# Kernel tuning notes

Hardware: AMD Instinct MI355X
Metric: run time of the kernel (lower is better)

Reference implementation:

```python
import jax, jax.numpy as jnp
import numpy as np
from jax import lax

NQ = 5  # qubits
NL = 3  # circuit layers


def conv2d(x, w, b):
    y = lax.conv_general_dilated(x, w, (1, 1), 'SAME',
                                 dimension_numbers=('NCHW', 'OIHW', 'NCHW'))
    return y + b[None, :, None, None]


def batchnorm(x, g, b, eps=1e-5):
    # training-mode batch statistics over (N,H,W), matching nn.BatchNorm2d in train()
    mu = x.mean((0, 2, 3), keepdims=True)
    var = x.var((0, 2, 3), keepdims=True)
    return g[None, :, None, None] * (x - mu) * lax.rsqrt(var + eps) + b[None, :, None, None]


def maxpool2(x):
    return lax.reduce_window(x, -jnp.inf, lax.max, (1, 1, 2, 2), (1, 1, 2, 2), 'VALID')


def _apply_1q(state, U, w):
    # state: (2,)*NQ, wire w is axis w (PennyLane default.qubit ordering)
    s = jnp.tensordot(U, state, axes=([1], [w]))
    return jnp.moveaxis(s, 0, w)


def _cnot(state, c, t):
    s0 = jnp.take(state, 0, axis=c)
    s1 = jnp.take(state, 1, axis=c)
    ta = t if t < c else t - 1
    s1 = jnp.flip(s1, axis=ta)  # X on target when control=1
    return jnp.stack([s0, s1], axis=c)


def _rx(t):
    c, s = jnp.cos(t / 2), jnp.sin(t / 2)
    return jnp.array([[c, -1j * s], [-1j * s, c]], dtype=jnp.complex64)


def _ry(t):
    c, s = jnp.cos(t / 2), jnp.sin(t / 2)
    return jnp.array([[c, -s], [s, c]], dtype=jnp.complex64)


def _rz(t):
    e = jnp.exp(-1j * t / 2)
    z = jnp.zeros((), jnp.complex64)
    return jnp.array([[e, z], [z, jnp.conj(e)]], dtype=jnp.complex64)


def quantum_circuit(inputs, weights):
    # inputs: (5,), weights: (30,)  -> scalar <Z0 Z1 Z2>
    state = jnp.zeros((2,) * NQ, jnp.complex64).at[(0,) * NQ].set(1.0)
    npl = NQ * 2  # weights per layer = 10
    nw = weights.shape[0]
    for l in range(NL):
        for i in range(NQ):
            state = _apply_1q(state, _rx(inputs[i]), i)
        for i in range(NQ):
            state = _apply_1q(state, _ry(weights[(l * npl + i) % nw]), i)
            state = _apply_1q(state, _rz(weights[(l * npl + i + NQ) % nw]), i)
        for i in range(NQ - 1):
            state = _cnot(state, i, i + 1)
        state = _cnot(state, NQ - 1, 0)
    probs = jnp.abs(state) ** 2
    z = jnp.array([1.0, -1.0], jnp.float32)
    sign = z[:, None, None] * z[None, :, None] * z[None, None, :]  # Z on wires 0,1,2
    return jnp.sum(probs * sign[:, :, :, None, None])


def setup_inputs() -> dict:
    key = jax.random.key(0)
    ks = jax.random.split(key, 12)
    d = {}
    d['x'] = jax.random.normal(ks[0], (256, 1, 224, 224), jnp.float32)
    d['conv1_w'] = jax.random.normal(ks[1], (16, 1, 3, 3), jnp.float32) * 0.1
    d['conv1_b'] = jnp.zeros((16,), jnp.float32)
    d['bn1_g'] = jnp.ones((16,), jnp.float32)
    d['bn1_b'] = jnp.zeros((16,), jnp.float32)
    d['conv2_w'] = jax.random.normal(ks[2], (32, 16, 3, 3), jnp.float32) * 0.05
    d['conv2_b'] = jnp.zeros((32,), jnp.float32)
    d['bn2_g'] = jnp.ones((32,), jnp.float32)
    d['bn2_b'] = jnp.zeros((32,), jnp.float32)
    d['conv3_w'] = jax.random.normal(ks[3], (64, 32, 3, 3), jnp.float32) * 0.05
    d['conv3_b'] = jnp.zeros((64,), jnp.float32)
    d['bn3_g'] = jnp.ones((64,), jnp.float32)
    d['bn3_b'] = jnp.zeros((64,), jnp.float32)
    d['fc1_w'] = jax.random.normal(ks[4], (64, 5), jnp.float32) * 0.1   # (in,out)
    d['fc1_b'] = jnp.zeros((5,), jnp.float32)
    d['ln_g'] = jnp.ones((5,), jnp.float32)
    d['ln_b'] = jnp.zeros((5,), jnp.float32)
    d['q_params'] = jax.random.uniform(ks[5], (30,), jnp.float32)
    d['fc2_w'] = jax.random.normal(ks[6], (1, 32), jnp.float32) * 0.5
    d['fc2_b'] = jnp.zeros((32,), jnp.float32)
    d['fc3_w'] = jax.random.normal(ks[7], (32, 2), jnp.float32) * 0.2
    d['fc3_b'] = jnp.zeros((2,), jnp.float32)
    return d


def reference(x, conv1_w, conv1_b, bn1_g, bn1_b, conv2_w, conv2_b, bn2_g, bn2_b,
              conv3_w, conv3_b, bn3_g, bn3_b, fc1_w, fc1_b, ln_g, ln_b,
              q_params, fc2_w, fc2_b, fc3_w, fc3_b):
    h = maxpool2(jax.nn.relu(batchnorm(conv2d(x, conv1_w, conv1_b), bn1_g, bn1_b)))
    h = maxpool2(jax.nn.relu(batchnorm(conv2d(h, conv2_w, conv2_b), bn2_g, bn2_b)))
    h = maxpool2(jax.nn.relu(batchnorm(conv2d(h, conv3_w, conv3_b), bn3_g, bn3_b)))
    # dropout is identity in eval; adaptive avg pool (1,1) + flatten
    h = h.mean((2, 3))                    # (B, 64)
    h = h @ fc1_w + fc1_b                 # (B, 5)
    mu = h.mean(-1, keepdims=True)
    var = h.var(-1, keepdims=True)
    h = ln_g * (h - mu) * lax.rsqrt(var + 1e-5) + ln_b
    q = jax.vmap(lambda inp: quantum_circuit(inp, q_params))(h)  # (B,)
    q = q[:, None].astype(jnp.float32)    # (B, 1)
    h2 = jax.nn.relu(q @ fc2_w + fc2_b)   # (B, 32)
    logits = h2 @ fc3_w + fc3_b           # (B, 2)
    return jax.nn.log_softmax(logits, axis=1)
```

## Files before the change

kernel.cpp:

```cpp
#include <hip/hip_runtime.h>
#include <hip/hip_bf16.h>


typedef _Float16 f16;
typedef _Float16 f16x2 __attribute__((ext_vector_type(2)));
typedef _Float16 f16x4 __attribute__((ext_vector_type(4)));
typedef _Float16 f16x8 __attribute__((ext_vector_type(8)));
typedef float f32x4 __attribute__((ext_vector_type(4)));
typedef float f32x16 __attribute__((ext_vector_type(16)));

#define DEV static __device__ __forceinline__

DEV float wave_sum(float v) {
#pragma unroll
  for (int off = 32; off > 0; off >>= 1) v += __shfl_xor(v, off, 64);
  return v;
}

__global__ __launch_bounds__(256) void repack(const float* __restrict__ w2,
                                              const float* __restrict__ w3,
                                              f16* __restrict__ Bt2,
                                              f16* __restrict__ Bt3) {
  int t = blockIdx.x * 256 + threadIdx.x;
  int T = gridDim.x * 256;
  for (int i = t; i < 32 * 168; i += T) {
    int oc = i / 168, kk = i - oc * 168;
    float v = 0.f;
    if (kk < 144) {
      int tap = kk >> 4, ic = kk & 15;
      v = w2[(oc * 16 + ic) * 9 + tap];
    }
    Bt2[i] = (f16)v;
  }
  for (int i = t; i < 64 * 296; i += T) {
    int oc = i / 296, kk = i - oc * 296;
    float v = 0.f;
    if (kk < 288) {
      int tap = kk / 32, ic = kk & 31;
      v = w3[(oc * 32 + ic) * 9 + tap];
    }
    Bt3[i] = (f16)v;
  }
}

__global__ __launch_bounds__(64) void finalize(const float* __restrict__ banks,
                                               const float* __restrict__ g,
                                               const float* __restrict__ b,
                                               float* __restrict__ scsh, int C,
                                               float inv_n) {
  int c = blockIdx.x, bk = threadIdx.x;
  float s = banks[bk * 2 * C + c];
  float qq = banks[bk * 2 * C + C + c];
  s = wave_sum(s);
  qq = wave_sum(qq);
  if (bk == 0) {
    float mean = s * inv_n;
    float var = qq * inv_n - mean * mean;
    float sc = g[c] * rsqrtf(var + 1e-5f);
    scsh[c] = sc;
    scsh[C + c] = b[c] - mean * sc;
  }
}

__global__ __launch_bounds__(256) void l1_mfma32(const float* __restrict__ x,
                                                 const float* __restrict__ w1,
                                                 float* __restrict__ banks,
                                                 f16* __restrict__ h1raw) {
  __shared__ f16 xA[18 * 240];
  __shared__ f16 xB[18 * 240];
  __shared__ f16 lrow[4 * 3616];
  __shared__ float lstat[32];
  int bid = blockIdx.x;
  int n = bid / 14, band = bid - n * 14;
  int y0 = band * 16;
  int t = threadIdx.x;
  if (t < 32) lstat[t] = 0.f;
  for (int i = t; i < 1008; i += 256) {
    int r = i / 56, k = i - r * 56;
    int y = y0 - 1 + r;
    float4 v = make_float4(0.f, 0.f, 0.f, 0.f);
    if ((unsigned)y < 224u)
      v = *(const float4*)(x + ((size_t)(n * 224 + y)) * 224 + k * 4);
    f16 h0 = (f16)v.x, h1 = (f16)v.y, h2 = (f16)v.z, h3 = (f16)v.w;
    f16* pa = xA + r * 240 + 4 * k + 1;
    pa[0] = h0; pa[1] = h1; pa[2] = h2; pa[3] = h3;
    f16x4 pk = {h0, h1, h2, h3};
    *(f16x4*)(xB + r * 240 + 4 * k) = pk;
  }
  if (t < 18) {
    xA[t * 240 + 0] = (f16)0.f;
    xA[t * 240 + 225] = (f16)0.f;
    xA[t * 240 + 226] = (f16)0.f;
    xB[t * 240 + 224] = (f16)0.f;
    xB[t * 240 + 225] = (f16)0.f;
  }
  __syncthreads();

  int wave = t >> 6, lane = t & 63;
  int g = lane >> 5, m32 = lane & 31;
  int oc = m32 & 15, s = m32 >> 4;

  f16x8 b;
#pragma unroll
  for (int j = 0; j < 8; j++) {
    int ky = 2 * g + (j >> 2), kx = j & 3;
    int kys = ky - s;
    float wv = 0.f;
    if (kx < 3 && kys >= 0 && kys < 3) wv = w1[oc * 9 + kys * 3 + kx];
    b[j] = (f16)wv;
  }

  const f16* abase = (m32 & 1) ? (xB + (m32 - 1)) : (xA + m32);
  f16* myrow = lrow + wave * 3616;
  f16* mrow = myrow + s * 1808;
  f32x16 zero16;
#pragma unroll
  for (int r = 0; r < 16; r++) zero16[r] = 0.f;
  const int bp[8] = {0, 1, 4, 5, 8, 9, 12, 13};
  float ssum = 0.f, ssq = 0.f;

  for (int rp = wave; rp < 8; rp += 4) {
    int r0 = 2 * rp + 2 * g;
    const f16* rbase = abase + r0 * 240;
#pragma unroll
    for (int xt = 0; xt < 7; xt++) {
      const f16* p0 = rbase + xt * 32;
      f16x2 v0 = *(const f16x2*)(p0);
      f16x2 v1 = *(const f16x2*)(p0 + 2);
      f16x2 v2 = *(const f16x2*)(p0 + 240);
      f16x2 v3 = *(const f16x2*)(p0 + 242);
      f16x8 a = {v0[0], v0[1], v1[0], v1[1], v2[0], v2[1], v3[0], v3[1]};
      f32x16 acc = __builtin_amdgcn_mfma_f32_32x32x16_f16(a, b, zero16, 0, 0, 0);
#pragma unroll
      for (int r = 0; r < 16; r++) {
        float v = acc[r];
        ssum += v;
        ssq += v * v;
      }
#pragma unroll
      for (int i = 0; i < 8; i++) {
        float pm = fmaxf(acc[2 * i], acc[2 * i + 1]);
        int pxp = xt * 16 + bp[i] + 2 * g;
        mrow[pxp * 16 + oc] = (f16)pm;
      }
    }
    int ph = band * 8 + rp;
    f16* gdst = h1raw + ((size_t)(n * 112) + ph) * 112 * 16;
    for (int i = lane; i < 224; i += 64) {
      f16x8 va = *(const f16x8*)(myrow + i * 8);
      f16x8 vb = *(const f16x8*)(myrow + 1808 + i * 8);
#pragma unroll
      for (int k = 0; k < 8; k++) va[k] = (va[k] > vb[k]) ? va[k] : vb[k];
      *(f16x8*)(gdst + i * 8) = va;
    }
  }
  ssum += __shfl_xor(ssum, 16, 64);
  ssum += __shfl_xor(ssum, 32, 64);
  ssq += __shfl_xor(ssq, 16, 64);
  ssq += __shfl_xor(ssq, 32, 64);
  if (lane < 16) {
    atomicAdd(&lstat[oc], ssum);
    atomicAdd(&lstat[16 + oc], ssq);
  }
  __syncthreads();
  if (t < 32) atomicAdd(&banks[(bid & 63) * 32 + t], lstat[t]);
}

__global__ __launch_bounds__(256, 2) void l2_gemm(
    const f16* __restrict__ h1, const f16* __restrict__ Btg,
    const float* __restrict__ scsh1, f16* __restrict__ p2,
    float* __restrict__ banks) {
  extern __shared__ char smem[];
  f16* lin0 = (f16*)smem;
  f16* lin1 = (f16*)(smem + 32832);
  f16* lpool = (f16*)(smem + 65664);
  float* lstat = (float*)(smem + 72832);
  int bid = blockIdx.x;
  int n = bid / 7, sb = bid - n * 7;
  int t = threadIdx.x;
  int wave = t >> 6, lane = t & 63, q = lane >> 4, wi = lane & 15;
  const int icq = (q & 1) * 8;

  f16x8 breg0[5], breg1[5];
#pragma unroll
  for (int j = 0; j < 5; j++) {
    breg0[j] = *(const f16x8*)(Btg + wi * 168 + j * 32 + q * 8);
    breg1[j] = *(const f16x8*)(Btg + (16 + wi) * 168 + j * 32 + q * 8);
  }

  f16x8 L[6];
  {
    int gb4 = sb * 16;
#pragma unroll
    for (int k = 0; k < 6; k++) {
      int i = t + k * 256;
      f16x8 v = {0, 0, 0, 0, 0, 0, 0, 0};
      if (i < 1344) {
        int r = i / 224, c = i - r * 224;
        int y = gb4 + r - 1;
        if ((unsigned)y < 112u)
          v = *(const f16x8*)(h1 + ((size_t)(n * 112 + y)) * 112 * 16 + c * 8);
      }
      L[k] = v;
    }
  }
  __builtin_amdgcn_sched_barrier(0);
  if (t < 64) lstat[t] = 0.f;
  if (t < 48) {
    f16* dst = (t < 24) ? lin0 : lin1;
    int tt = (t < 24) ? t : t - 24;
    int r = tt >> 2, k2 = tt & 3;
    f16x8 z = {0, 0, 0, 0, 0, 0, 0, 0};
    int pos = (k2 < 2) ? 0 : 113;
    *(f16x8*)(dst + (r * 114 + pos) * 24 + (k2 & 1) * 8) = z;
  }
  {
    int gb4 = sb * 16;
#pragma unroll
    for (int k = 0; k < 6; k++) {
      int i = t + k * 256;
      if (i < 1344) {
        int r = i / 224, c = i - r * 224;
        int y = gb4 + r - 1;
        f16x8 o = {0, 0, 0, 0, 0, 0, 0, 0};
        if ((unsigned)y < 112u) {
          f16x8 xv = L[k];
          int ch0 = (c & 1) * 8;
#pragma unroll
          for (int e = 0; e < 8; e++) {
            float f = (float)xv[e] * scsh1[ch0 + e] + scsh1[16 + ch0 + e];
            o[e] = (f16)fmaxf(f, 0.f);
          }
        }
        *(f16x8*)(lin0 + (r * 114 + 1 + (c >> 1)) * 24 + (c & 1) * 8) = o;
      }
    }
  }
  __syncthreads();

  float tS0 = 0.f, tQ0 = 0.f, tS1 = 0.f, tQ1 = 0.f;
  f16* cur = lin0;
  f16* nxt = lin1;

  for (int b = 0; b < 4; b++) {
    int gb = sb * 4 + b;
    if (b < 3) {
      int gb4 = (gb + 1) * 4;
#pragma unroll
      for (int k = 0; k < 6; k++) {
        int i = t + k * 256;
        f16x8 v = {0, 0, 0, 0, 0, 0, 0, 0};
        if (i < 1344) {
          int r = i / 224, c = i - r * 224;
          int y = gb4 + r - 1;
          if ((unsigned)y < 112u)
            v = *(const f16x8*)(h1 +
                                ((size_t)(n * 112 + y)) * 112 * 16 + c * 8);
        }
        L[k] = v;
      }
      __builtin_amdgcn_sched_barrier(0);
    }

    f32x4 acc[7][2];
#pragma unroll
    for (int f = 0; f < 7; f++)
#pragma unroll
      for (int nf = 0; nf < 2; nf++)
#pragma unroll
        for (int r = 0; r < 4; r++) acc[f][nf][r] = 0.f;

#pragma unroll
    for (int j = 0; j < 5; j++) {
      const int tA = 2 * j, tB = 2 * j + 1;
      const int kyA = tA / 3, kxA = tA % 3;
      const int kyB = (tB < 9) ? tB / 3 : 0, kxB = (tB < 9) ? tB % 3 : 0;
      bool hiq = (q >= 2);
      int ky = hiq ? kyB : kyA;
      int kx = hiq ? kxB : kxA;
      const f16* aptr0 = cur + ((wave + ky) * 114 + wi + kx) * 24 + icq;
      f16x8 b0 = breg0[j];
      f16x8 b1 = breg1[j];
#pragma unroll
      for (int f = 0; f < 7; f++) {
        f16x8 a = *(const f16x8*)(aptr0 + f * 384);
        acc[f][0] =
            __builtin_amdgcn_mfma_f32_16x16x32_f16(a, b0, acc[f][0], 0, 0, 0);
        acc[f][1] =
            __builtin_amdgcn_mfma_f32_16x16x32_f16(a, b1, acc[f][1], 0, 0, 0);
      }
    }

#pragma unroll
    for (int f = 0; f < 7; f++)
#pragma unroll
      for (int r = 0; r < 4; r++) {
        float v0 = acc[f][0][r], v1 = acc[f][1][r];
        tS0 += v0; tQ0 += v0 * v0;
        tS1 += v1; tQ1 += v1 * v1;
      }

    if (wave & 1) {
#pragma unroll
      for (int f = 0; f < 7; f++)
#pragma unroll
        for (int nf = 0; nf < 2; nf++) {
          int ch = nf * 16 + wi;
          int pc0 = f * 8 + q * 2;
          float m0 = fmaxf(acc[f][nf][0], acc[f][nf][1]);
          float m1 = fmaxf(acc[f][nf][2], acc[f][nf][3]);
          lpool[((wave >> 1) * 56 + pc0) * 32 + ch] = (f16)m0;
          lpool[((wave >> 1) * 56 + pc0 + 1) * 32 + ch] = (f16)m1;
        }
    }

    if (b < 3) {
      int gb4 = (gb + 1) * 4;
#pragma unroll
      for (int k = 0; k < 6; k++) {
        int i = t + k * 256;
        if (i < 1344) {
          int r = i / 224, c = i - r * 224;
          int y = gb4 + r - 1;
          f16x8 o = {0, 0, 0, 0, 0, 0, 0, 0};
          if ((unsigned)y < 112u) {
            f16x8 xv = L[k];
            int ch0 = (c & 1) * 8;
#pragma unroll
            for (int e = 0; e < 8; e++) {
              float f = (float)xv[e] * scsh1[ch0 + e] + scsh1[16 + ch0 + e];
              o[e] = (f16)fmaxf(f, 0.f);
            }
          }
          *(f16x8*)(nxt + (r * 114 + 1 + (c >> 1)) * 24 + (c & 1) * 8) = o;
        }
      }
    }
    __syncthreads();

    if (!(wave & 1)) {
      int ph = gb * 2 + (wave >> 1);
#pragma unroll
      for (int f = 0; f < 7; f++)
#pragma unroll
        for (int nf = 0; nf < 2; nf++) {
          int ch = nf * 16 + wi;
          int pc0 = f * 8 + q * 2;
          float m0 = fmaxf(acc[f][nf][0], acc[f][nf][1]);
          float m1 = fmaxf(acc[f][nf][2], acc[f][nf][3]);
          m0 = fmaxf(m0, (float)lpool[((wave >> 1) * 56 + pc0) * 32 + ch]);
          m1 = fmaxf(m1, (float)lpool[((wave >> 1) * 56 + pc0 + 1) * 32 + ch]);
          size_t ob = (((size_t)n * 56 + ph) * 56) * 32;
          p2[ob + (size_t)pc0 * 32 + ch] = (f16)m0;
          p2[ob + (size_t)(pc0 + 1) * 32 + ch] = (f16)m1;
        }
    }
    __syncthreads();

    f16* tmpp = cur; cur = nxt; nxt = tmpp;
  }

  tS0 += __shfl_xor(tS0, 16, 64); tS0 += __shfl_xor(tS0, 32, 64);
  tQ0 += __shfl_xor(tQ0, 16, 64); tQ0 += __shfl_xor(tQ0, 32, 64);
  tS1 += __shfl_xor(tS1, 16, 64); tS1 += __shfl_xor(tS1, 32, 64);
  tQ1 += __shfl_xor(tQ1, 16, 64); tQ1 += __shfl_xor(tQ1, 32, 64);
  if (q == 0) {
    atomicAdd(&lstat[wi], tS0);
    atomicAdd(&lstat[16 + wi], tS1);
    atomicAdd(&lstat[32 + wi], tQ0);
    atomicAdd(&lstat[48 + wi], tQ1);
  }
  __syncthreads();
  if (t < 64) {
    int i = t >> 5, c = t & 31;
    atomicAdd(&banks[(bid & 63) * 64 + i * 32 + c], lstat[i * 32 + c]);
  }
}

__global__ __launch_bounds__(256) void l3_gemm(const f16* __restrict__ p2,
                                               const f16* __restrict__ Btg,
                                               const float* __restrict__ scsh2,
                                               f16* __restrict__ p3,
                                               float* __restrict__ banks) {
  extern __shared__ char smem[];
  f16* lin = (f16*)smem;
  float* lstat = (float*)(smem + 27840);
  f16* lpool = (f16*)smem;
  int bx = blockIdx.x;
  int n = bx / 14, band = bx - n * 14, h0 = band * 4;
  int t = threadIdx.x;
  int wave = t >> 6, lane = t & 63, q = lane >> 4, wi = lane & 15;
  int mhalf = wave & 1, nfpair = wave >> 1;
  f16x8 breg0[9], breg1[9];
#pragma unroll
  for (int j = 0; j < 9; j++) {
    breg0[j] = *(const f16x8*)(Btg + (nfpair * 32 + wi) * 296 + j * 32 + q * 8);
    breg1[j] =
        *(const f16x8*)(Btg + (nfpair * 32 + 16 + wi) * 296 + j * 32 + q * 8);
  }
  if (t < 128) lstat[t] = 0.f;
  {
    for (int i = t; i < 1344; i += 256) {
      int r = i / 224, rem = i - r * 224;
      int c = rem >> 2, cp = rem & 3;
      int y = h0 + r - 1;
      f16x8 o = {0, 0, 0, 0, 0, 0, 0, 0};
      if ((unsigned)y < 56u) {
        const f16* src = p2 + (((size_t)(n * 56 + y)) * 56 + c) * 32 + cp * 8;
        f16x8 xv = *(const f16x8*)src;
        int ch0 = cp * 8;
#pragma unroll
        for (int k = 0; k < 8; k++) {
          float f = (float)xv[k] * scsh2[ch0 + k] + scsh2[32 + ch0 + k];
          o[k] = (f16)fmaxf(f, 0.f);
        }
      }
      *(f16x8*)(lin + (r * 58 + 1 + c) * 40 + cp * 8) = o;
    }
    if (t < 48) {
      int r = t / 8, k = t & 7;
      int col = (k < 4) ? 0 : 57, cp = k & 3;
      f16x8 z = {0, 0, 0, 0, 0, 0, 0, 0};
      *(f16x8*)(lin + (r * 58 + col) * 40 + cp * 8) = z;
    }
  }
  __syncthreads();
  int abase[7];
#pragma unroll
  for (int f = 0; f < 7; f++) {
    int pos = mhalf * 112 + f * 16 + wi;
    int r = pos / 56, w = pos - r * 56;
    abase[f] = (r * 58 + w) * 40 + q * 8;
  }
  f32x4 acc[7][2];
#pragma unroll
  for (int f = 0; f < 7; f++)
#pragma unroll
    for (int nf = 0; nf < 2; nf++)
#pragma unroll
      for (int r = 0; r < 4; r++) acc[f][nf][r] = 0.f;

#pragma unroll
  for (int j = 0; j < 9; j++) {
    const int ky = j / 3, kx = j % 3;
    f16x8 b0 = breg0[j];
    f16x8 b1 = breg1[j];
#pragma unroll
    for (int f = 0; f < 7; f++) {
      f16x8 a = *(const f16x8*)(lin + abase[f] + (ky * 58 + kx) * 40);
      acc[f][0] = __builtin_amdgcn_mfma_f32_16x16x32_f16(a, b0, acc[f][0], 0, 0, 0);
      acc[f][1] = __builtin_amdgcn_mfma_f32_16x16x32_f16(a, b1, acc[f][1], 0, 0, 0);
    }
  }
  int ch0 = nfpair * 32 + wi, ch1 = ch0 + 16;
  float s0 = 0.f, q0 = 0.f, s1 = 0.f, q1 = 0.f;
#pragma unroll
  for (int f = 0; f < 7; f++)
#pragma unroll
    for (int r = 0; r < 4; r++) {
      float v0 = acc[f][0][r], v1 = acc[f][1][r];
      s0 += v0; q0 += v0 * v0;
      s1 += v1; q1 += v1 * v1;
    }
  s0 += __shfl_xor(s0, 16, 64); s0 += __shfl_xor(s0, 32, 64);
  q0 += __shfl_xor(q0, 16, 64); q0 += __shfl_xor(q0, 32, 64);
  s1 += __shfl_xor(s1, 16, 64); s1 += __shfl_xor(s1, 32, 64);
  q1 += __shfl_xor(q1, 16, 64); q1 += __shfl_xor(q1, 32, 64);
  if (q == 0) {
    atomicAdd(&lstat[ch0], s0);
    atomicAdd(&lstat[ch1], s1);
    atomicAdd(&lstat[64 + ch0], q0);
    atomicAdd(&lstat[64 + ch1], q1);
  }
  __syncthreads();
#pragma unroll
  for (int f = 0; f < 7; f++) {
    int pos = mhalf * 112 + f * 16 + q * 4;
    int r0 = pos / 56, w0 = pos - r0 * 56;
#pragma unroll
    for (int nf = 0; nf < 2; nf++) {
      int ch = nf ? ch1 : ch0;
      float m0 = fmaxf(acc[f][nf][0], acc[f][nf][1]);
      float m1 = fmaxf(acc[f][nf][2], acc[f][nf][3]);
      lpool[(r0 * 28 + (w0 >> 1)) * 64 + ch] = (f16)m0;
      lpool[(r0 * 28 + (w0 >> 1) + 1) * 64 + ch] = (f16)m1;
    }
  }
  __syncthreads();
  for (int i = t; i < 3584; i += 256) {
    int ch = i & 63, rest = i >> 6;
    int pc = rest % 28, pr = rest / 28;
    float v = fmaxf((float)lpool[((2 * pr) * 28 + pc) * 64 + ch],
                    (float)lpool[((2 * pr + 1) * 28 + pc) * 64 + ch]);
    int gpr = band * 2 + pr;
    p3[(((size_t)n * 28 + gpr) * 28 + pc) * 64 + ch] = (f16)v;
  }
  if (t < 128) {
    atomicAdd(&banks[(bx & 63) * 128 + t], lstat[t]);
  }
}

__global__ __launch_bounds__(256) void head_pool(
    const f16* __restrict__ p3, const float* __restrict__ scsh3,
    const float* __restrict__ fc1w, const float* __restrict__ fc1b,
    float* __restrict__ featg) {
  int n = blockIdx.x, t = threadIdx.x;
  __shared__ float red[64 * 33];
  __shared__ float meanc[64];
  int oct = t & 7, strip = t >> 3;
  float sc[8], sh[8];
#pragma unroll
  for (int k = 0; k < 8; k++) {
    sc[k] = scsh3[oct * 8 + k];
    sh[k] = scsh3[64 + oct * 8 + k];
  }
  float acc[8];
#pragma unroll
  for (int k = 0; k < 8; k++) acc[k] = 0.f;
  const f16* base = p3 + (size_t)n * 50176 + oct * 8;
  for (int px = strip; px < 784; px += 32) {
    f16x8 v = *(const f16x8*)(base + (size_t)px * 64);
#pragma unroll
    for (int k = 0; k < 8; k++)
      acc[k] += fmaxf((float)v[k] * sc[k] + sh[k], 0.f);
  }
#pragma unroll
  for (int k = 0; k < 8; k++) red[(oct * 8 + k) * 33 + strip] = acc[k];
  __syncthreads();
  if (t < 64) {
    float s = 0.f;
    for (int j = 0; j < 32; j++) s += red[t * 33 + j];
    meanc[t] = s * (1.f / 784.f);
  }
  __syncthreads();
  if (t < 5) {
    float a = fc1b[t];
    for (int i = 0; i < 64; i++) a += meanc[i] * fc1w[i * 5 + t];
    featg[n * 8 + t] = a;
  }
}

template <int W>
DEV void g_rx(float (&sr)[32], float (&si)[32], float c, float s) {
  constexpr int m = 1 << (4 - W);
#pragma unroll
  for (int i0 = 0; i0 < 32; i0++)
    if (!(i0 & m)) {
      int i1 = i0 | m;
      float a0r = sr[i0], a0i = si[i0], a1r = sr[i1], a1i = si[i1];
      sr[i0] = c * a0r + s * a1i;
      si[i0] = c * a0i - s * a1r;
      sr[i1] = s * a0i + c * a1r;
      si[i1] = -s * a0r + c * a1i;
    }
}

template <int W>
DEV void g_ry(float (&sr)[32], float (&si)[32], float c, float s) {
  constexpr int m = 1 << (4 - W);
#pragma unroll
  for (int i0 = 0; i0 < 32; i0++)
    if (!(i0 & m)) {
      int i1 = i0 | m;
      float a0r = sr[i0], a0i = si[i0], a1r = sr[i1], a1i = si[i1];
      sr[i0] = c * a0r - s * a1r;
      si[i0] = c * a0i - s * a1i;
      sr[i1] = s * a0r + c * a1r;
      si[i1] = s * a0i + c * a1i;
    }
}

template <int W>
DEV void g_rz(float (&sr)[32], float (&si)[32], float c, float s) {
  constexpr int m = 1 << (4 - W);
#pragma unroll
  for (int i0 = 0; i0 < 32; i0++)
    if (!(i0 & m)) {
      int i1 = i0 | m;
      float a0r = sr[i0], a0i = si[i0], a1r = sr[i1], a1i = si[i1];
      sr[i0] = c * a0r + s * a0i;
      si[i0] = c * a0i - s * a0r;
      sr[i1] = c * a1r - s * a1i;
      si[i1] = c * a1i + s * a1r;
    }
}

template <int C, int T>
DEV void g_cnot(float (&sr)[32], float (&si)[32]) {
  constexpr int mc = 1 << (4 - C), mt = 1 << (4 - T);
#pragma unroll
  for (int i0 = 0; i0 < 32; i0++)
    if ((i0 & mc) && !(i0 & mt)) {
      int i1 = i0 | mt;
      float tr = sr[i0]; sr[i0] = sr[i1]; sr[i1] = tr;
      float ti = si[i0]; si[i0] = si[i1]; si[i1] = ti;
    }
}

__global__ __launch_bounds__(64) void head_q(
    const float* __restrict__ featg, const float* __restrict__ lng,
    const float* __restrict__ lnb, const float* __restrict__ qp,
    const float* __restrict__ fc2w, const float* __restrict__ fc2b,
    const float* __restrict__ fc3w, const float* __restrict__ fc3b,
    float* __restrict__ out) {
  int n = blockIdx.x * 64 + threadIdx.x;
  float f[5];
#pragma unroll
  for (int i = 0; i < 5; i++) f[i] = featg[n * 8 + i];
  float mu = (f[0] + f[1] + f[2] + f[3] + f[4]) * 0.2f;
  float var = 0.f;
#pragma unroll
  for (int i = 0; i < 5; i++) { float d = f[i] - mu; var += d * d; }
  var *= 0.2f;
  float inv = rsqrtf(var + 1e-5f);
#pragma unroll
  for (int i = 0; i < 5; i++) f[i] = lng[i] * (f[i] - mu) * inv + lnb[i];

  float cx[5], sx[5];
#pragma unroll
  for (int i = 0; i < 5; i++) {
    cx[i] = cosf(0.5f * f[i]);
    sx[i] = sinf(0.5f * f[i]);
  }
  float sr[32], si[32];
#pragma unroll
  for (int i = 0; i < 32; i++) { sr[i] = 0.f; si[i] = 0.f; }
  sr[0] = 1.f;

  for (int l = 0; l < 3; l++) {
    g_rx<0>(sr, si, cx[0], sx[0]);
    g_rx<1>(sr, si, cx[1], sx[1]);
    g_rx<2>(sr, si, cx[2], sx[2]);
    g_rx<3>(sr, si, cx[3], sx[3]);
    g_rx<4>(sr, si, cx[4], sx[4]);
#define WIRE_YZ(I)                                             \
  {                                                            \
    float ty = qp[l * 10 + I];                                 \
    g_ry<I>(sr, si, cosf(0.5f * ty), sinf(0.5f * ty));         \
    float tz = qp[l * 10 + I + 5];                             \
    g_rz<I>(sr, si, cosf(0.5f * tz), sinf(0.5f * tz));         \
  }
    WIRE_YZ(0) WIRE_YZ(1) WIRE_YZ(2) WIRE_YZ(3) WIRE_YZ(4)
#undef WIRE_YZ
    g_cnot<0, 1>(sr, si);
    g_cnot<1, 2>(sr, si);
    g_cnot<2, 3>(sr, si);
    g_cnot<3, 4>(sr, si);
    g_cnot<4, 0>(sr, si);
  }
  float qv = 0.f;
#pragma unroll
  for (int idx = 0; idx < 32; idx++) {
    float p = sr[idx] * sr[idx] + si[idx] * si[idx];
    qv += (__popc(idx & 0x1C) & 1) ? -p : p;
  }
  float l0 = fc3b[0], l1 = fc3b[1];
  for (int j = 0; j < 32; j++) {
    float hv = fmaxf(qv * fc2w[j] + fc2b[j], 0.f);
    l0 += hv * fc3w[j * 2];
    l1 += hv * fc3w[j * 2 + 1];
  }
  float mx = fmaxf(l0, l1);
  float lse = mx + logf(expf(l0 - mx) + expf(l1 - mx));
  out[n * 2 + 0] = l0 - lse;
  out[n * 2 + 1] = l1 - lse;
}

extern "C" void kernel_launch(void* const* d_in, const int* in_sizes, int n_in,
                              void* d_out, int out_size, void* d_ws,
                              size_t ws_size, hipStream_t stream) {
  const float* x    = (const float*)d_in[0];
  const float* w1   = (const float*)d_in[1];
  const float* bn1g = (const float*)d_in[3];
  const float* bn1b = (const float*)d_in[4];
  const float* w2   = (const float*)d_in[5];
  const float* bn2g = (const float*)d_in[7];
  const float* bn2b = (const float*)d_in[8];
  const float* w3   = (const float*)d_in[9];
  const float* bn3g = (const float*)d_in[11];
  const float* bn3b = (const float*)d_in[12];
  const float* fc1w = (const float*)d_in[13];
  const float* fc1b = (const float*)d_in[14];
  const float* lng  = (const float*)d_in[15];
  const float* lnb  = (const float*)d_in[16];
  const float* qp   = (const float*)d_in[17];
  const float* fc2w = (const float*)d_in[18];
  const float* fc2b = (const float*)d_in[19];
  const float* fc3w = (const float*)d_in[20];
  const float* fc3b = (const float*)d_in[21];
  float* out = (float*)d_out;

  char* ws = (char*)d_ws;
  float* banks1 = (float*)ws;
  float* banks2 = (float*)(ws + 8192);
  float* banks3 = (float*)(ws + 24576);
  float* scsh1 = (float*)(ws + 57344);
  float* scsh2 = (float*)(ws + 57472);
  float* scsh3 = (float*)(ws + 57728);
  f16* Bt2 = (f16*)(ws + 58240);
  f16* Bt3 = (f16*)(ws + 68992);
  f16* h1 = (f16*)(ws + 106880);
  f16* p2 = (f16*)(ws + 106880 + 102760448ULL);
  f16* p3 = (f16*)(ws + 106880 + 102760448ULL + 51380224ULL);
  float* featg = banks2;

  hipMemsetAsync(ws, 0, 57344, stream);
  repack<<<16, 256, 0, stream>>>(w2, w3, Bt2, Bt3);
  l1_mfma32<<<3584, 256, 0, stream>>>(x, w1, banks1, h1);
  finalize<<<16, 64, 0, stream>>>(banks1, bn1g, bn1b, scsh1, 16,
                                  1.f / 12845056.f);
  l2_gemm<<<1792, 256, 73088, stream>>>(h1, Bt2, scsh1, p2, banks2);
  finalize<<<32, 64, 0, stream>>>(banks2, bn2g, bn2b, scsh2, 32,
                                  1.f / 3211264.f);
  l3_gemm<<<3584, 256, 28352, stream>>>(p2, Bt3, scsh2, p3, banks3);
  finalize<<<64, 64, 0, stream>>>(banks3, bn3g, bn3b, scsh3, 64,
                                  1.f / 802816.f);
  head_pool<<<256, 256, 0, stream>>>(p3, scsh3, fc1w, fc1b, featg);
  head_q<<<4, 64, 0, stream>>>(featg, lng, lnb, qp, fc2w, fc2b, fc3w, fc3b,
                               out);
}
```

Baseline: 357.8 us.

## Make l3_gemm persistent over seven bands with double-buffered LDS prefetch

The layer-3 conv kernel now launches 512 blocks, each covering half an image (seven 4-row bands), instead of one block per band. The next band's input is loaded into registers before the MFMA loop and written into a second LDS buffer afterwards, so global loads overlap compute. Weight register loads and the BN-stat atomics are paid once per block instead of once per band. In exchange each block uses more LDS and adds extra barriers per band, and the grid is coarser with launch bounds set to two blocks per SIMD group.

```diff
diff --git a/kernel.cpp b/kernel.cpp
--- a/kernel.cpp
+++ b/kernel.cpp
@@ -377,20 +377,22 @@
   }
 }
 
-__global__ __launch_bounds__(256) void l3_gemm(const f16* __restrict__ p2,
-                                               const f16* __restrict__ Btg,
-                                               const float* __restrict__ scsh2,
-                                               f16* __restrict__ p3,
-                                               float* __restrict__ banks) {
+__global__ __launch_bounds__(256, 2) void l3_gemm(
+    const f16* __restrict__ p2, const f16* __restrict__ Btg,
+    const float* __restrict__ scsh2, f16* __restrict__ p3,
+    float* __restrict__ banks) {
   extern __shared__ char smem[];
-  f16* lin = (f16*)smem;
-  float* lstat = (float*)(smem + 27840);
-  f16* lpool = (f16*)smem;
+  f16* lin0 = (f16*)smem;
+  f16* lin1 = (f16*)(smem + 27840);
+  f16* lpool = (f16*)(smem + 55680);
+  float* lstat = (float*)(smem + 70016);
   int bx = blockIdx.x;
-  int n = bx / 14, band = bx - n * 14, h0 = band * 4;
+  int n = bx >> 1, sb = bx & 1;
   int t = threadIdx.x;
   int wave = t >> 6, lane = t & 63, q = lane >> 4, wi = lane & 15;
   int mhalf = wave & 1, nfpair = wave >> 1;
+  int ch0 = nfpair * 32 + wi, ch1 = ch0 + 16;
+
   f16x8 breg0[9], breg1[9];
 #pragma unroll
   for (int j = 0; j < 9; j++) {
@@ -398,33 +400,61 @@
     breg1[j] =
         *(const f16x8*)(Btg + (nfpair * 32 + 16 + wi) * 296 + j * 32 + q * 8);
   }
+
+  f16x8 L[6];
+  {
+    int yb = sb * 28;
+#pragma unroll
+    for (int k = 0; k < 6; k++) {
+      int i = t + k * 256;
+      f16x8 v = {0, 0, 0, 0, 0, 0, 0, 0};
+      if (i < 1344) {
+        int r = i / 224, rem = i - r * 224;
+        int c = rem >> 2, cp = rem & 3;
+        int y = yb + r - 1;
+        if ((unsigned)y < 56u)
+          v = *(const f16x8*)(p2 + (((size_t)(n * 56 + y)) * 56 + c) * 32 +
+                              cp * 8);
+      }
+      L[k] = v;
+    }
+  }
+  __builtin_amdgcn_sched_barrier(0);
   if (t < 128) lstat[t] = 0.f;
+  if (t < 96) {
+    f16* dst = (t < 48) ? lin0 : lin1;
+    int tt = (t < 48) ? t : t - 48;
+    int r = tt / 8, k = tt & 7;
+    int col = (k < 4) ? 0 : 57, cp = k & 3;
+    f16x8 z = {0, 0, 0, 0, 0, 0, 0, 0};
+    *(f16x8*)(dst + (r * 58 + col) * 40 + cp * 8) = z;
+  }
   {
-    for (int i = t; i < 1344; i += 256) {
-      int r = i / 224, rem = i - r * 224;
-      int c = rem >> 2, cp = rem & 3;
-      int y = h0 + r - 1;
-      f16x8 o = {0, 0, 0, 0, 0, 0, 0, 0};
-      if ((unsigned)y < 56u) {
-        const f16* src = p2 + (((size_t)(n * 56 + y)) * 56 + c) * 32 + cp * 8;
-        f16x8 xv = *(const f16x8*)src;
-        int ch0 = cp * 8;
-#pragma unroll
-        for (int k = 0; k < 8; k++) {
-          float f = (float)xv[k] * scsh2[ch0 + k] + scsh2[32 + ch0 + k];
-          o[k] = (f16)fmaxf(f, 0.f);
+    int yb = sb * 28;
+#pragma unroll
+    for (int k = 0; k < 6; k++) {
+      int i = t + k * 256;
+      if (i < 1344) {
+        int r = i / 224, rem = i - r * 224;
+        int c = rem >> 2, cp = rem & 3;
+        int y = yb + r - 1;
+        f16x8 o = {0, 0, 0, 0, 0, 0, 0, 0};
+        if ((unsigned)y < 56u) {
+          f16x8 xv = L[k];
+          int che = cp * 8;
+#pragma unroll
+          for (int e = 0; e < 8; e++) {
+            float f = (float)xv[e] * scsh2[che + e] + scsh2[32 + che + e];
+            o[e] = (f16)fmaxf(f, 0.f);
+          }
         }
-      }
-      *(f16x8*)(lin + (r * 58 + 1 + c) * 40 + cp * 8) = o;
-    }
-    if (t < 48) {
-      int r = t / 8, k = t & 7;
-      int col = (k < 4) ? 0 : 57, cp = k & 3;
-      f16x8 z = {0, 0, 0, 0, 0, 0, 0, 0};
-      *(f16x8*)(lin + (r * 58 + col) * 40 + cp * 8) = z;
+        *(f16x8*)(lin0 + (r * 58 + 1 + c) * 40 + cp * 8) = o;
+      }
     }
   }
   __syncthreads();
+
+  float tS0 = 0.f, tQ0 = 0.f, tS1 = 0.f, tQ1 = 0.f;
   int abase[7];
 #pragma unroll
   for (int f = 0; f < 7; f++) {
@@ -432,69 +462,125 @@
     int r = pos / 56, w = pos - r * 56;
     abase[f] = (r * 58 + w) * 40 + q * 8;
   }
-  f32x4 acc[7][2];
-#pragma unroll
-  for (int f = 0; f < 7; f++)
-#pragma unroll
-    for (int nf = 0; nf < 2; nf++)
-#pragma unroll
-      for (int r = 0; r < 4; r++) acc[f][nf][r] = 0.f;
-
-#pragma unroll
-  for (int j = 0; j < 9; j++) {
-    const int ky = j / 3, kx = j % 3;
-    f16x8 b0 = breg0[j];
-    f16x8 b1 = breg1[j];
+  f16* cur = lin0;
+  f16* nxt = lin1;
+
+  for (int b = 0; b < 7; b++) {
+    int gb = sb * 7 + b;
+    if (b < 6) {
+      int yb = (gb + 1) * 4;
+#pragma unroll
+      for (int k = 0; k < 6; k++) {
+        int i = t + k * 256;
+        f16x8 v = {0, 0, 0, 0, 0, 0, 0, 0};
+        if (i < 1344) {
+          int r = i / 224, rem = i - r * 224;
+          int c = rem >> 2, cp = rem & 3;
+          int y = yb + r - 1;
+          if ((unsigned)y < 56u)
+            v = *(const f16x8*)(p2 + (((size_t)(n * 56 + y)) * 56 + c) * 32 +
+                                cp * 8);
+        }
+        L[k] = v;
+      }
+      __builtin_amdgcn_sched_barrier(0);
+    }
+
+    f32x4 acc[7][2];
+#pragma unroll
+    for (int f = 0; f < 7; f++)
+#pragma unroll
+      for (int nf = 0; nf < 2; nf++)
+#pragma unroll
+        for (int r = 0; r < 4; r++) acc[f][nf][r] = 0.f;
+
+#pragma unroll
+    for (int j = 0; j < 9; j++) {
+      const int ky = j / 3, kx = j % 3;
+      f16x8 b0 = breg0[j];
+      f16x8 b1 = breg1[j];
+#pragma unroll
+      for (int f = 0; f < 7; f++) {
+        f16x8 a = *(const f16x8*)(cur + abase[f] + (ky * 58 + kx) * 40);
+        acc[f][0] =
+            __builtin_amdgcn_mfma_f32_16x16x32_f16(a, b0, acc[f][0], 0, 0, 0);
+        acc[f][1] =
+            __builtin_amdgcn_mfma_f32_16x16x32_f16(a, b1, acc[f][1], 0, 0, 0);
+      }
+    }
+
+#pragma unroll
+    for (int f = 0; f < 7; f++)
+#pragma unroll
+      for (int r = 0; r < 4; r++) {
+        float v0 = acc[f][0][r], v1 = acc[f][1][r];
+        tS0 += v0; tQ0 += v0 * v0;
+        tS1 += v1; tQ1 += v1 * v1;
+      }
+
 #pragma unroll
     for (int f = 0; f < 7; f++) {
-      f16x8 a = *(const f16x8*)(lin + abase[f] + (ky * 58 + kx) * 40);
-      acc[f][0] = __builtin_amdgcn_mfma_f32_16x16x32_f16(a, b0, acc[f][0], 0, 0, 0);
-      acc[f][1] = __builtin_amdgcn_mfma_f32_16x16x32_f16(a, b1, acc[f][1], 0, 0, 0);
-    }
-  }
-  int ch0 = nfpair * 32 + wi, ch1 = ch0 + 16;
-  float s0 = 0.f, q0 = 0.f, s1 = 0.f, q1 = 0.f;
-#pragma unroll
-  for (int f = 0; f < 7; f++)
-#pragma unroll
-    for (int r = 0; r < 4; r++) {
-      float v0 = acc[f][0][r], v1 = acc[f][1][r];
-      s0 += v0; q0 += v0 * v0;
-      s1 += v1; q1 += v1 * v1;
-    }
-  s0 += __shfl_xor(s0, 16, 64); s0 += __shfl_xor(s0, 32, 64);
-  q0 += __shfl_xor(q0, 16, 64); q0 += __shfl_xor(q0, 32, 64);
-  s1 += __shfl_xor(s1, 16, 64); s1 += __shfl_xor(s1, 32, 64);
-  q1 += __shfl_xor(q1, 16, 64); q1 += __shfl_xor(q1, 32, 64);
+      int pos = mhalf * 112 + f * 16 + q * 4;
+      int r0 = pos / 56, w0 = pos - r0 * 56;
+#pragma unroll
+      for (int nf = 0; nf < 2; nf++) {
+        int ch = nf ? ch1 : ch0;
+        float m0 = fmaxf(acc[f][nf][0], acc[f][nf][1]);
+        float m1 = fmaxf(acc[f][nf][2], acc[f][nf][3]);
+        lpool[(r0 * 28 + (w0 >> 1)) * 64 + ch] = (f16)m0;
+        lpool[(r0 * 28 + (w0 >> 1) + 1) * 64 + ch] = (f16)m1;
+      }
+    }
+
+    if (b < 6) {
+      int yb = (gb + 1) * 4;
+#pragma unroll
+      for (int k = 0; k < 6; k++) {
+        int i = t + k * 256;
+        if (i < 1344) {
+          int r = i / 224, rem = i - r * 224;
+          int c = rem >> 2, cp = rem & 3;
+          int y = yb + r - 1;
+          f16x8 o = {0, 0, 0, 0, 0, 0, 0, 0};
+          if ((unsigned)y < 56u) {
+            f16x8 xv = L[k];
+            int che = cp * 8;
+#pragma unroll
+            for (int e = 0; e < 8; e++) {
+              float f = (float)xv[e] * scsh2[che + e] + scsh2[32 + che + e];
+              o[e] = (f16)fmaxf(f, 0.f);
+            }
+          }
+          *(f16x8*)(nxt + (r * 58 + 1 + c) * 40 + cp * 8) = o;
+        }
+      }
+    }
+    __syncthreads();
+
+    for (int i = t; i < 3584; i += 256) {
+      int ch = i & 63, rest = i >> 6;
+      int pc = rest % 28, pr = rest / 28;
+      float v = fmaxf((float)lpool[((2 * pr) * 28 + pc) * 64 + ch],
+                      (float)lpool[((2 * pr + 1) * 28 + pc) * 64 + ch]);
+      int gpr = gb * 2 + pr;
+      p3[(((size_t)n * 28 + gpr) * 28 + pc) * 64 + ch] = (f16)v;
+    }
+    __syncthreads();
+
+    f16* tmpp = cur; cur = nxt; nxt = tmpp;
+  }
+
+  tS0 += __shfl_xor(tS0, 16, 64); tS0 += __shfl_xor(tS0, 32, 64);
+  tQ0 += __shfl_xor(tQ0, 16, 64); tQ0 += __shfl_xor(tQ0, 32, 64);
+  tS1 += __shfl_xor(tS1, 16, 64); tS1 += __shfl_xor(tS1, 32, 64);
+  tQ1 += __shfl_xor(tQ1, 16, 64); tQ1 += __shfl_xor(tQ1, 32, 64);
   if (q == 0) {
-    atomicAdd(&lstat[ch0], s0);
-    atomicAdd(&lstat[ch1], s1);
-    atomicAdd(&lstat[64 + ch0], q0);
-    atomicAdd(&lstat[64 + ch1], q1);
+    atomicAdd(&lstat[ch0], tS0);
+    atomicAdd(&lstat[ch1], tS1);
+    atomicAdd(&lstat[64 + ch0], tQ0);
+    atomicAdd(&lstat[64 + ch1], tQ1);
   }
   __syncthreads();
-#pragma unroll
-  for (int f = 0; f < 7; f++) {
-    int pos = mhalf * 112 + f * 16 + q * 4;
-    int r0 = pos / 56, w0 = pos - r0 * 56;
-#pragma unroll
-    for (int nf = 0; nf < 2; nf++) {
-      int ch = nf ? ch1 : ch0;
-      float m0 = fmaxf(acc[f][nf][0], acc[f][nf][1]);
-      float m1 = fmaxf(acc[f][nf][2], acc[f][nf][3]);
-      lpool[(r0 * 28 + (w0 >> 1)) * 64 + ch] = (f16)m0;
-      lpool[(r0 * 28 + (w0 >> 1) + 1) * 64 + ch] = (f16)m1;
-    }
-  }
-  __syncthreads();
-  for (int i = t; i < 3584; i += 256) {
-    int ch = i & 63, rest = i >> 6;
-    int pc = rest % 28, pr = rest / 28;
-    float v = fmaxf((float)lpool[((2 * pr) * 28 + pc) * 64 + ch],
-                    (float)lpool[((2 * pr + 1) * 28 + pc) * 64 + ch]);
-    int gpr = band * 2 + pr;
-    p3[(((size_t)n * 28 + gpr) * 28 + pc) * 64 + ch] = (f16)v;
-  }
   if (t < 128) {
     atomicAdd(&banks[(bx & 63) * 128 + t], lstat[t]);
   }
@@ -712,7 +798,7 @@
   l2_gemm<<<1792, 256, 73088, stream>>>(h1, Bt2, scsh1, p2, banks2);
   finalize<<<32, 64, 0, stream>>>(banks2, bn2g, bn2b, scsh2, 32,
                                   1.f / 3211264.f);
-  l3_gemm<<<3584, 256, 28352, stream>>>(p2, Bt3, scsh2, p3, banks3);
+  l3_gemm<<<512, 256, 70528, stream>>>(p2, Bt3, scsh2, p3, banks3);
   finalize<<<64, 64, 0, stream>>>(banks3, bn3g, bn3b, scsh3, 64,
                                   1.f / 802816.f);
   head_pool<<<256, 256, 0, stream>>>(p3, scsh3, fc1w, fc1b, featg);
```

Result: no change. 362.6 us (+1.4%).

## Double l3_gemm row band per block, each wave computing all 64 output channels

Applied to the files above, without the earlier changes.

Each l3_gemm block now processes 8 input rows (4 pooled output rows) instead of 4, halving the grid. Each wave covers a 112-position slice across all 64 output channels and keeps all 36 B fragments in registers, so each A fragment loaded from LDS feeds 4 MFMAs instead of 2. The aim is to cut halo reloads and LDS A-traffic per MFMA and amortize per-block setup. The cost is much higher register pressure (36 f16x8 B regs plus 28 accumulators), larger LDS per block, fewer blocks, and launch_bounds(256,2), which may cause spills or reduce occupancy.

```diff
diff --git a/kernel.cpp b/kernel.cpp
--- a/kernel.cpp
+++ b/kernel.cpp
@@ -377,122 +377,133 @@
   }
 }
 
-__global__ __launch_bounds__(256) void l3_gemm(const f16* __restrict__ p2,
-                                               const f16* __restrict__ Btg,
-                                               const float* __restrict__ scsh2,
-                                               f16* __restrict__ p3,
-                                               float* __restrict__ banks) {
+__global__ __launch_bounds__(256, 2) void l3_gemm(
+    const f16* __restrict__ p2, const f16* __restrict__ Btg,
+    const float* __restrict__ scsh2, f16* __restrict__ p3,
+    float* __restrict__ banks) {
   extern __shared__ char smem[];
   f16* lin = (f16*)smem;
-  float* lstat = (float*)(smem + 27840);
+  float* lstat = (float*)(smem + 46400);
   f16* lpool = (f16*)smem;
   int bx = blockIdx.x;
-  int n = bx / 14, band = bx - n * 14, h0 = band * 4;
+  int n = bx / 7, sb = bx - n * 7;
   int t = threadIdx.x;
   int wave = t >> 6, lane = t & 63, q = lane >> 4, wi = lane & 15;
-  int mhalf = wave & 1, nfpair = wave >> 1;
-  f16x8 breg0[9], breg1[9];
-#pragma unroll
-  for (int j = 0; j < 9; j++) {
-    breg0[j] = *(const f16x8*)(Btg + (nfpair * 32 + wi) * 296 + j * 32 + q * 8);
-    breg1[j] =
-        *(const f16x8*)(Btg + (nfpair * 32 + 16 + wi) * 296 + j * 32 + q * 8);
-  }
+
+  f16x8 breg[9][4];
+#pragma unroll
+  for (int j = 0; j < 9; j++)
+#pragma unroll
+    for (int h = 0; h < 4; h++)
+      breg[j][h] =
+          *(const f16x8*)(Btg + (h * 16 + wi) * 296 + j * 32 + q * 8);
+
   if (t < 128) lstat[t] = 0.f;
-  {
-    for (int i = t; i < 1344; i += 256) {
+#pragma unroll
+  for (int k = 0; k < 9; k++) {
+    int i = t + k * 256;
+    if (i < 2240) {
       int r = i / 224, rem = i - r * 224;
       int c = rem >> 2, cp = rem & 3;
-      int y = h0 + r - 1;
+      int y = sb * 8 + r - 1;
       f16x8 o = {0, 0, 0, 0, 0, 0, 0, 0};
       if ((unsigned)y < 56u) {
-        const f16* src = p2 + (((size_t)(n * 56 + y)) * 56 + c) * 32 + cp * 8;
-        f16x8 xv = *(const f16x8*)src;
+        f16x8 xv =
+            *(const f16x8*)(p2 + (((size_t)(n * 56 + y)) * 56 + c) * 32 +
+                            cp * 8);
         int ch0 = cp * 8;
 #pragma unroll
-        for (int k = 0; k < 8; k++) {
-          float f = (float)xv[k] * scsh2[ch0 + k] + scsh2[32 + ch0 + k];
-          o[k] = (f16)fmaxf(f, 0.f);
+        for (int e = 0; e < 8; e++) {
+          float f = (float)xv[e] * scsh2[ch0 + e] + scsh2[32 + ch0 + e];
+          o[e] = (f16)fmaxf(f, 0.f);
         }
       }
       *(f16x8*)(lin + (r * 58 + 1 + c) * 40 + cp * 8) = o;
     }
-    if (t < 48) {
-      int r = t / 8, k = t & 7;
-      int col = (k < 4) ? 0 : 57, cp = k & 3;
-      f16x8 z = {0, 0, 0, 0, 0, 0, 0, 0};
-      *(f16x8*)(lin + (r * 58 + col) * 40 + cp * 8) = z;
-    }
-  }
-  __syncthreads();
+  }
+  if (t < 80) {
+    int r = t / 8, k = t & 7;
+    int col = (k < 4) ? 0 : 57, cp = k & 3;
+    f16x8 z = {0, 0, 0, 0, 0, 0, 0, 0};
+    *(f16x8*)(lin + (r * 58 + col) * 40 + cp * 8) = z;
+  }
+  __syncthreads();
+
   int abase[7];
 #pragma unroll
   for (int f = 0; f < 7; f++) {
-    int pos = mhalf * 112 + f * 16 + wi;
+    int pos = wave * 112 + f * 16 + wi;
     int r = pos / 56, w = pos - r * 56;
     abase[f] = (r * 58 + w) * 40 + q * 8;
   }
-  f32x4 acc[7][2];
+  f32x4 acc[7][4];
 #pragma unroll
   for (int f = 0; f < 7; f++)
 #pragma unroll
-    for (int nf = 0; nf < 2; nf++)
-#pragma unroll
-      for (int r = 0; r < 4; r++) acc[f][nf][r] = 0.f;
+    for (int h = 0; h < 4; h++)
+#pragma unroll
+      for (int r = 0; r < 4; r++) acc[f][h][r] = 0.f;
 
 #pragma unroll
   for (int j = 0; j < 9; j++) {
     const int ky = j / 3, kx = j % 3;
-    f16x8 b0 = breg0[j];
-    f16x8 b1 = breg1[j];
 #pragma unroll
     for (int f = 0; f < 7; f++) {
       f16x8 a = *(const f16x8*)(lin + abase[f] + (ky * 58 + kx) * 40);
-      acc[f][0] = __builtin_amdgcn_mfma_f32_16x16x32_f16(a, b0, acc[f][0], 0, 0, 0);
-      acc[f][1] = __builtin_amdgcn_mfma_f32_16x16x32_f16(a, b1, acc[f][1], 0, 0, 0);
-    }
-  }
-  int ch0 = nfpair * 32 + wi, ch1 = ch0 + 16;
-  float s0 = 0.f, q0 = 0.f, s1 = 0.f, q1 = 0.f;
+#pragma unroll
+      for (int h = 0; h < 4; h++)
+        acc[f][h] =
+            __builtin_amdgcn_mfma_f32_16x16x32_f16(a, breg[j][h], acc[f][h],
+                                                   0, 0, 0);
+    }
+  }
+
+  float tS[4] = {0.f, 0.f, 0.f, 0.f}, tQ[4] = {0.f, 0.f, 0.f, 0.f};
 #pragma unroll
   for (int f = 0; f < 7; f++)
 #pragma unroll
-    for (int r = 0; r < 4; r++) {
-      float v0 = acc[f][0][r], v1 = acc[f][1][r];
-      s0 += v0; q0 += v0 * v0;
-      s1 += v1; q1 += v1 * v1;
-    }
-  s0 += __shfl_xor(s0, 16, 64); s0 += __shfl_xor(s0, 32, 64);
-  q0 += __shfl_xor(q0, 16, 64); q0 += __shfl_xor(q0, 32, 64);
-  s1 += __shfl_xor(s1, 16, 64); s1 += __shfl_xor(s1, 32, 64);
-  q1 += __shfl_xor(q1, 16, 64); q1 += __shfl_xor(q1, 32, 64);
+    for (int h = 0; h < 4; h++)
+#pragma unroll
+      for (int r = 0; r < 4; r++) {
+        float v = acc[f][h][r];
+        tS[h] += v;
+        tQ[h] += v * v;
+      }
+#pragma unroll
+  for (int h = 0; h < 4; h++) {
+    tS[h] += __shfl_xor(tS[h], 16, 64); tS[h] += __shfl_xor(tS[h], 32, 64);
+    tQ[h] += __shfl_xor(tQ[h], 16, 64); tQ[h] += __shfl_xor(tQ[h], 32, 64);
+  }
   if (q == 0) {
-    atomicAdd(&lstat[ch0], s0);
-    atomicAdd(&lstat[ch1], s1);
-    atomicAdd(&lstat[64 + ch0], q0);
-    atomicAdd(&lstat[64 + ch1], q1);
-  }
-  __syncthreads();
+#pragma unroll
+    for (int h = 0; h < 4; h++) {
+      atomicAdd(&lstat[h * 16 + wi], tS[h]);
+      atomicAdd(&lstat[64 + h * 16 + wi], tQ[h]);
+    }
+  }
+  __syncthreads();
+
 #pragma unroll
   for (int f = 0; f < 7; f++) {
-    int pos = mhalf * 112 + f * 16 + q * 4;
+    int pos = wave * 112 + f * 16 + q * 4;
     int r0 = pos / 56, w0 = pos - r0 * 56;
 #pragma unroll
-    for (int nf = 0; nf < 2; nf++) {
-      int ch = nf ? ch1 : ch0;
-      float m0 = fmaxf(acc[f][nf][0], acc[f][nf][1]);
-      float m1 = fmaxf(acc[f][nf][2], acc[f][nf][3]);
+    for (int h = 0; h < 4; h++) {
+      int ch = h * 16 + wi;
+      float m0 = fmaxf(acc[f][h][0], acc[f][h][1]);
+      float m1 = fmaxf(acc[f][h][2], acc[f][h][3]);
       lpool[(r0 * 28 + (w0 >> 1)) * 64 + ch] = (f16)m0;
       lpool[(r0 * 28 + (w0 >> 1) + 1) * 64 + ch] = (f16)m1;
     }
   }
   __syncthreads();
-  for (int i = t; i < 3584; i += 256) {
+
+  for (int i = t; i < 7168; i += 256) {
     int ch = i & 63, rest = i >> 6;
     int pc = rest % 28, pr = rest / 28;
     float v = fmaxf((float)lpool[((2 * pr) * 28 + pc) * 64 + ch],
                     (float)lpool[((2 * pr + 1) * 28 + pc) * 64 + ch]);
-    int gpr = band * 2 + pr;
+    int gpr = sb * 4 + pr;
     p3[(((size_t)n * 28 + gpr) * 28 + pc) * 64 + ch] = (f16)v;
   }
   if (t < 128) {
@@ -712,7 +723,7 @@
   l2_gemm<<<1792, 256, 73088, stream>>>(h1, Bt2, scsh1, p2, banks2);
   finalize<<<32, 64, 0, stream>>>(banks2, bn2g, bn2b, scsh2, 32,
                                   1.f / 3211264.f);
-  l3_gemm<<<3584, 256, 28352, stream>>>(p2, Bt3, scsh2, p3, banks3);
+  l3_gemm<<<1792, 256, 46912, stream>>>(p2, Bt3, scsh2, p3, banks3);
   finalize<<<64, 64, 0, stream>>>(banks3, bn3g, bn3b, scsh3, 64,
                                   1.f / 802816.f);
   head_pool<<<256, 256, 0, stream>>>(p3, scsh3, fc1w, fc1b, featg);
```

Result: no change. 351.7 us (-1.7%).
